# Performance work log

Measured on AMD Instinct MI355X. Metric: run time of the kernel, lower is better.

The kernel has to match this reference:

```python
import jax, jax.numpy as jnp
import numpy as np

B, N, DIN, DH, DOUT, H = 64, 512, 256, 512, 256, 4


def setup_inputs() -> dict:
    key = jax.random.key(0)
    ks = jax.random.split(key, 11)
    s = 0.02
    return {
        "x": jax.random.normal(ks[0], (B, N, DIN), jnp.float32),
        # block 0 (in=DIN): per-head embed Linear(DIN,DH) and KQ Linear(DIN,2*DH)
        "e_w0": jax.random.normal(ks[1], (H, DIN, DH), jnp.float32) * s,
        "e_b0": jax.random.normal(ks[2], (H, DH), jnp.float32) * s,
        "kq_w0": jax.random.normal(ks[3], (H, DIN, 2 * DH), jnp.float32) * s,
        "kq_b0": jax.random.normal(ks[4], (H, 2 * DH), jnp.float32) * s,
        # block 1 (in=DH)
        "e_w1": jax.random.normal(ks[5], (H, DH, DH), jnp.float32) * s,
        "e_b1": jax.random.normal(ks[6], (H, DH), jnp.float32) * s,
        "kq_w1": jax.random.normal(ks[7], (H, DH, 2 * DH), jnp.float32) * s,
        "kq_b1": jax.random.normal(ks[8], (H, 2 * DH), jnp.float32) * s,
        # output projection Linear(DH, DOUT)
        "proj_w": jax.random.normal(ks[9], (DH, DOUT), jnp.float32) * s,
        "proj_b": jax.random.normal(ks[10], (DOUT,), jnp.float32) * s,
    }


def _multi_attn(x, ew, eb, kqw, kqb):
    # x: [b,n,d]; ew: [h,d,e]; kqw: [h,d,2e]. num_hidden_layers=2 => each MLP is one Linear.
    embs = jnp.einsum('bnd,hde->hbne', x, ew) + eb[:, None, None, :]
    kq = jnp.einsum('bnd,hdf->hbnf', x, kqw) + kqb[:, None, None, :]
    K, Q = jnp.split(kq, 2, axis=-1)  # torch.chunk order: K first, then Q
    A = jax.nn.softmax(jnp.einsum('hbqe,hbke->hbqk', Q, K), axis=-1)  # unscaled
    out = jnp.einsum('hbqk,hbke->hbqe', A, embs)
    return out.mean(axis=0)  # mean over heads


def reference(x, e_w0, e_b0, kq_w0, kq_b0, e_w1, e_b1, kq_w1, kq_b1, proj_w, proj_b):
    h = _multi_attn(x, e_w0, e_b0, kq_w0, kq_b0)
    h = _multi_attn(h, e_w1, e_b1, kq_w1, kq_b1)
    return h @ proj_w + proj_b
```

## Files before the change

### kernel.cpp

```cpp
#include <hip/hip_runtime.h>

typedef _Float16 half8 __attribute__((ext_vector_type(8)));
typedef _Float16 half4 __attribute__((ext_vector_type(4)));
typedef float floatx4 __attribute__((ext_vector_type(4)));

#define B_    64
#define N_    512
#define DIN_  256
#define DH_   512
#define DOUT_ 256
#define H_    4
#define BN_   (B_ * N_)

#define WAIT_VM4_LGKM0() __builtin_amdgcn_s_waitcnt(0x0074)
#define WAIT_VM0_LGKM0() __builtin_amdgcn_s_waitcnt(0x0070)
#define WAIT_VM4()       __builtin_amdgcn_s_waitcnt(0x0F74)
#define WAIT_VM0()       __builtin_amdgcn_s_waitcnt(0x0F70)
#define MEMBAR()         __asm__ __volatile__("" ::: "memory")
#define BAR()            do { MEMBAR(); __builtin_amdgcn_s_barrier(); MEMBAR(); } while (0)

__device__ static inline void async_copy16(const _Float16* g, _Float16* l) {
    __builtin_amdgcn_global_load_lds(
        (const __attribute__((address_space(1))) void*)g,
        (__attribute__((address_space(3))) void*)l, 16, 0, 0);
}

template <bool OUT_F16>
__global__ __launch_bounds__(256)
void gemm_f16(const _Float16* __restrict__ A, long long aS1, long long aS2, int lda, long long aSeg,
              const _Float16* __restrict__ B, long long bS1, long long bS2, int ldb, long long bSeg,
              void* __restrict__ Cv, long long cS1, long long cS2, int ldc,
              int K, const float* __restrict__ bias, int biasMode,
              long long biasS1, long long biasS2, int zShift)
{
    __shared__ __align__(16) _Float16 As[3][128 * 32];
    __shared__ __align__(16) _Float16 Bs[3][128 * 32];

    const int tid  = threadIdx.x;
    const int wave = tid >> 6;
    const int lane = tid & 63;
    const int quad = lane >> 4;
    const int r16  = lane & 15;

    const int z  = blockIdx.z;
    const int z1 = z >> zShift;
    const int z2 = z & ((1 << zShift) - 1);

    const int gx = gridDim.x, gy = gridDim.y;
    const int T = gx * gy;
    int lin = blockIdx.y * gx + blockIdx.x;
    int id2 = (T & 7) ? lin : ((lin & 7) * (T >> 3) + (lin >> 3));
    const int m0 = (id2 / gx) * 128;
    const int n0 = (id2 % gx) * 128;

    const int srow = lane >> 2;
    const int scol = (((lane & 3) ^ ((lane >> 3) & 3))) * 8;

    const _Float16* gaRow = A + z1 * aS1 + z2 * aS2
                              + (long long)(m0 + wave * 32 + srow) * lda + scol;
    const _Float16* gbRow = B + z1 * bS1 + z2 * bS2
                              + (long long)(n0 + wave * 32 + srow) * ldb + scol;

    const int wm = (wave >> 1) * 64;
    const int wn = (wave & 1) * 64;
    const int gl = (quad ^ ((r16 >> 1) & 3)) * 8;

    floatx4 acc[4][4];
#pragma unroll
    for (int i = 0; i < 4; i++)
#pragma unroll
        for (int j = 0; j < 4; j++) acc[i][j] = (floatx4){0.f, 0.f, 0.f, 0.f};

    auto stage = [&](int p, int k0) {
        const _Float16* a = gaRow + (long long)(k0 >> 9) * aSeg + (k0 & 511);
        const _Float16* b = gbRow + (long long)(k0 >> 9) * bSeg + (k0 & 511);
        _Float16* la = &As[p][wave * 1024];
        _Float16* lb = &Bs[p][wave * 1024];
        async_copy16(a,                    la);
        async_copy16(a + (size_t)16 * lda, la + 512);
        async_copy16(b,                    lb);
        async_copy16(b + (size_t)16 * ldb, lb + 512);
    };

    auto compute = [&](int p) {
        half8 af[4], bf[4];
#pragma unroll
        for (int i = 0; i < 4; i++)
            af[i] = *(const half8*)&As[p][(wm + i * 16 + r16) * 32 + gl];
#pragma unroll
        for (int j = 0; j < 4; j++)
            bf[j] = *(const half8*)&Bs[p][(wn + j * 16 + r16) * 32 + gl];
#pragma unroll
        for (int i = 0; i < 4; i++)
#pragma unroll
            for (int j = 0; j < 4; j++)
                acc[i][j] = __builtin_amdgcn_mfma_f32_16x16x32_f16(
                    bf[j], af[i], acc[i][j], 0, 0, 0);
    };

    const int niter = K >> 5;
    stage(0, 0);
    stage(1, 32);
    int pNext = 2;
    int pCur  = 0;
    for (int it = 0; it < niter - 1; ++it) {
        MEMBAR(); WAIT_VM4_LGKM0();
        __builtin_amdgcn_s_barrier();
        MEMBAR();
        if (it + 2 < niter) stage(pNext, (it + 2) << 5);
        compute(pCur);
        MEMBAR();
        pNext = (pNext == 2) ? 0 : pNext + 1;
        pCur  = (pCur  == 2) ? 0 : pCur  + 1;
    }
    MEMBAR(); WAIT_VM0_LGKM0();
    __builtin_amdgcn_s_barrier(); MEMBAR();
    compute(pCur);

    const float* bz = bias + z1 * biasS1 + z2 * biasS2;
    float*    Cf = (float*)Cv    + z1 * cS1 + z2 * cS2;
    _Float16* Ch = (_Float16*)Cv + z1 * cS1 + z2 * cS2;
#pragma unroll
    for (int i = 0; i < 4; i++) {
        const int row = m0 + wm + i * 16 + r16;
#pragma unroll
        for (int j = 0; j < 4; j++) {
            const int col = n0 + wn + j * 16 + quad * 4;
            float v0 = acc[i][j][0], v1 = acc[i][j][1],
                  v2 = acc[i][j][2], v3 = acc[i][j][3];
            if (biasMode == 1) {
                v0 += bz[col]; v1 += bz[col + 1];
                v2 += bz[col + 2]; v3 += bz[col + 3];
            } else if (biasMode == 2) {
                const float bv = bz[row];
                v0 += bv; v1 += bv; v2 += bv; v3 += bv;
            }
            const size_t idx = (size_t)row * ldc + col;
            if (OUT_F16) {
                half4 hv = {(_Float16)v0, (_Float16)v1, (_Float16)v2, (_Float16)v3};
                *(half4*)&Ch[idx] = hv;
            } else {
                float4 fv = {v0, v1, v2, v3};
                *(float4*)&Cf[idx] = fv;
            }
        }
    }
}

template <bool OUT_F16>
__global__ __launch_bounds__(512, 2)
void gemm256(const _Float16* __restrict__ A, long long aS1, long long aS2, int lda, long long aSeg, int aSh,
             const _Float16* __restrict__ B, long long bS1, long long bS2, int ldb, long long bSeg, int bSh,
             void* __restrict__ Cv, long long cS1, long long cS2, int ldc,
             int K, const float* __restrict__ bias, int biasMode,
             long long biasS1, long long biasS2, int zShift)
{
    extern __shared__ __align__(16) _Float16 lds[];
    _Float16* AsB = lds;
    _Float16* BsB = lds + 2 * 256 * 64;

    const int tid  = threadIdx.x;
    const int wave = tid >> 6;
    const int lane = tid & 63;
    const int quad = lane >> 4;
    const int r16  = lane & 15;
    const int wr   = wave >> 2;
    const int wc   = wave & 3;

    const int z  = blockIdx.z;
    const int z1 = z >> zShift;
    const int z2 = z & ((1 << zShift) - 1);

    const int aTSh = aSh - 6, aTMk = (1 << aTSh) - 1;
    const int bTSh = bSh - 6, bTMk = (1 << bTSh) - 1;

    const int gx = gridDim.x, gy = gridDim.y;
    const int T = gx * gy;
    int lin = blockIdx.y * gx + blockIdx.x;
    int id2 = (T & 7) ? lin : ((lin & 7) * (T >> 3) + (lin >> 3));
    const int m0 = (id2 / gx) * 256;
    const int n0 = (id2 % gx) * 256;

    const int sr  = tid >> 3;
    const int swz = ((tid & 7) ^ (sr & 7)) * 8;
    const _Float16* gaA = A + z1 * aS1 + z2 * aS2 + (long long)(m0 + sr) * lda + swz;
    const _Float16* gbB = B + z1 * bS1 + z2 * bS2 + (long long)(n0 + sr) * ldb + swz;

    const int arow = wr * 64 + r16;
    const int brow = wc * 32 + r16;
    const int rsw  = r16 & 7;
    const int gxk0 = (quad ^ rsw) * 8;
    const int gxk1 = ((4 + quad) ^ rsw) * 8;

    floatx4 acc[8][4];
#pragma unroll
    for (int i = 0; i < 8; i++)
#pragma unroll
        for (int j = 0; j < 4; j++) acc[i][j] = (floatx4){0.f, 0.f, 0.f, 0.f};

    half8 af[4][2], bf0s[2][2], bf1s[2][2];

    auto stageA = [&](int buf, int h, int tt2) {
        const _Float16* s = gaA + (long long)(h * 128) * lda
                          + (long long)(tt2 >> aTSh) * aSeg + ((tt2 & aTMk) << 6);
        _Float16* d = AsB + buf * 16384 + h * 8192 + wave * 512;
        async_copy16(s, d);
        async_copy16(s + (long long)64 * lda, d + 4096);
    };
    auto stageB = [&](int buf, int h, int tt2) {
        const _Float16* s = gbB + (long long)(h * 128) * ldb
                          + (long long)(tt2 >> bTSh) * bSeg + ((tt2 & bTMk) << 6);
        _Float16* d = BsB + buf * 16384 + h * 8192 + wave * 512;
        async_copy16(s, d);
        async_copy16(s + (long long)64 * ldb, d + 4096);
    };

#define LOAD_AF(RH, BUF) do { \
    const _Float16* ab_ = AsB + (BUF) * 16384 + ((RH) * 128 + arow) * 64; \
    _Pragma("unroll") \
    for (int i5 = 0; i5 < 4; i5++) { \
        af[i5][0] = *(const half8*)(ab_ + i5 * 1024 + gxk0); \
        af[i5][1] = *(const half8*)(ab_ + i5 * 1024 + gxk1); \
    } \
} while (0)

#define LOAD_BF(DST, CH, BUF) do { \
    const _Float16* bb_ = BsB + (BUF) * 16384 + ((CH) * 128 + brow) * 64; \
    _Pragma("unroll") \
    for (int j5 = 0; j5 < 2; j5++) { \
        DST[j5][0] = *(const half8*)(bb_ + j5 * 1024 + gxk0); \
        DST[j5][1] = *(const half8*)(bb_ + j5 * 1024 + gxk1); \
    } \
} while (0)

#define MFMA16(RH, CH, BFS) do { \
    _Pragma("unroll") \
    for (int i6 = 0; i6 < 4; i6++) { \
        _Pragma("unroll") \
        for (int j6 = 0; j6 < 2; j6++) { \
            floatx4 c_ = acc[(RH) * 4 + i6][(CH) * 2 + j6]; \
            c_ = __builtin_amdgcn_mfma_f32_16x16x32_f16(BFS[j6][0], af[i6][0], c_, 0, 0, 0); \
            c_ = __builtin_amdgcn_mfma_f32_16x16x32_f16(BFS[j6][1], af[i6][1], c_, 0, 0, 0); \
            acc[(RH) * 4 + i6][(CH) * 2 + j6] = c_; \
        } \
    } \
} while (0)

    const int nit = K >> 7;

    stageA(0, 0, 0);
    stageB(0, 1, 0);
    stageA(0, 1, 0);
    stageB(0, 0, 0);
    stageA(1, 0, 1);
    stageB(1, 1, 1);
    WAIT_VM4();
    BAR();

    for (int it = 0; it < nit; ++it) {
        const int tt = it * 2;
        const bool full = (it < nit - 1);

        LOAD_AF(0, 0); LOAD_BF(bf0s, 0, 0);
        stageA(1, 1, tt + 1);
        BAR();
        __builtin_amdgcn_s_setprio(1); MFMA16(0, 0, bf0s); __builtin_amdgcn_s_setprio(0);
        BAR();
        LOAD_BF(bf1s, 1, 0);
        stageB(1, 0, tt + 1);
        BAR();
        __builtin_amdgcn_s_setprio(1); MFMA16(0, 1, bf1s); __builtin_amdgcn_s_setprio(0);
        BAR();
        LOAD_AF(1, 0);
        if (full) stageA(0, 0, tt + 2);
        BAR();
        __builtin_amdgcn_s_setprio(1); MFMA16(1, 1, bf1s); __builtin_amdgcn_s_setprio(0);
        BAR();
        if (full) stageB(0, 1, tt + 2);
        BAR();
        __builtin_amdgcn_s_setprio(1); MFMA16(1, 0, bf0s); __builtin_amdgcn_s_setprio(0);
        if (full) WAIT_VM4(); else WAIT_VM0();
        BAR();
        LOAD_AF(0, 1); LOAD_BF(bf0s, 0, 1);
        if (full) stageA(0, 1, tt + 2);
        BAR();
        __builtin_amdgcn_s_setprio(1); MFMA16(0, 0, bf0s); __builtin_amdgcn_s_setprio(0);
        BAR();
        LOAD_BF(bf1s, 1, 1);
        if (full) stageB(0, 0, tt + 2);
        BAR();
        __builtin_amdgcn_s_setprio(1); MFMA16(0, 1, bf1s); __builtin_amdgcn_s_setprio(0);
        BAR();
        LOAD_AF(1, 1);
        if (full) stageA(1, 0, tt + 3);
        BAR();
        __builtin_amdgcn_s_setprio(1); MFMA16(1, 1, bf1s); __builtin_amdgcn_s_setprio(0);
        BAR();
        if (full) stageB(1, 1, tt + 3);
        BAR();
        __builtin_amdgcn_s_setprio(1); MFMA16(1, 0, bf0s); __builtin_amdgcn_s_setprio(0);
        if (full) WAIT_VM4();
        BAR();
    }

#undef LOAD_AF
#undef LOAD_BF
#undef MFMA16

    const float* bz = bias + z1 * biasS1 + z2 * biasS2;
    float*    Cf = (float*)Cv    + z1 * cS1 + z2 * cS2;
    _Float16* Ch = (_Float16*)Cv + z1 * cS1 + z2 * cS2;
#pragma unroll
    for (int f = 0; f < 8; f++) {
        const int row = m0 + (f >> 2) * 128 + wr * 64 + (f & 3) * 16 + r16;
#pragma unroll
        for (int j = 0; j < 4; j++) {
            const int col = n0 + (j >> 1) * 128 + wc * 32 + (j & 1) * 16 + quad * 4;
            float v0 = acc[f][j][0], v1 = acc[f][j][1],
                  v2 = acc[f][j][2], v3 = acc[f][j][3];
            if (biasMode == 1) {
                v0 += bz[col]; v1 += bz[col + 1];
                v2 += bz[col + 2]; v3 += bz[col + 3];
            } else if (biasMode == 2) {
                const float bv = bz[row];
                v0 += bv; v1 += bv; v2 += bv; v3 += bv;
            }
            const size_t idx = (size_t)row * ldc + col;
            if (OUT_F16) {
                half4 hv = {(_Float16)v0, (_Float16)v1, (_Float16)v2, (_Float16)v3};
                *(half4*)&Ch[idx] = hv;
            } else {
                float4 fv = {v0, v1, v2, v3};
                *(float4*)&Cf[idx] = fv;
            }
        }
    }
}

__global__ __launch_bounds__(256)
void softmax_f16(_Float16* __restrict__ S)
{
    const int row  = blockIdx.x * 4 + (threadIdx.x >> 6);
    const int lane = threadIdx.x & 63;
    _Float16* s = S + (size_t)row * 512 + lane * 8;
    half8 h = *(const half8*)s;
    float v[8];
    float mx = -1e30f;
#pragma unroll
    for (int j = 0; j < 8; j++) { v[j] = (float)h[j]; mx = fmaxf(mx, v[j]); }
#pragma unroll
    for (int off = 32; off; off >>= 1) mx = fmaxf(mx, __shfl_xor(mx, off));
    float sum = 0.f;
#pragma unroll
    for (int j = 0; j < 8; j++) { v[j] = __expf(v[j] - mx); sum += v[j]; }
#pragma unroll
    for (int off = 32; off; off >>= 1) sum += __shfl_xor(sum, off);
    const float inv = 0.25f / sum;
#pragma unroll
    for (int j = 0; j < 8; j++) h[j] = (_Float16)(v[j] * inv);
    *(half8*)s = h;
}

__global__ __launch_bounds__(256)
void cvt_f32_f16(const float* __restrict__ in, _Float16* __restrict__ out)
{
    const size_t i = ((size_t)blockIdx.x * blockDim.x + threadIdx.x) * 4;
    const float4 f = *(const float4*)(in + i);
    out[i + 0] = (_Float16)f.x;
    out[i + 1] = (_Float16)f.y;
    out[i + 2] = (_Float16)f.z;
    out[i + 3] = (_Float16)f.w;
}

__global__ __launch_bounds__(256)
void transpose_cvt(const float* __restrict__ in, _Float16* __restrict__ out,
                   int R, int C)
{
    __shared__ float tile[32][33];
    const int g  = blockIdx.z;
    const int c0 = blockIdx.x * 32;
    const int r0 = blockIdx.y * 32;
    const float* inp  = in  + (size_t)g * R * C;
    _Float16*    outp = out + (size_t)g * R * C;
#pragma unroll
    for (int i = threadIdx.y; i < 32; i += 8)
        tile[i][threadIdx.x] = inp[(size_t)(r0 + i) * C + c0 + threadIdx.x];
    __syncthreads();
#pragma unroll
    for (int i = threadIdx.y; i < 32; i += 8)
        outp[(size_t)(c0 + i) * R + r0 + threadIdx.x] = (_Float16)tile[threadIdx.x][i];
}

__global__ __launch_bounds__(256)
void wk_bq(const float* __restrict__ kq_w, const float* __restrict__ kq_b,
           float* __restrict__ w, int dinShift)
{
    const int t = blockIdx.x * 256 + threadIdx.x;
    const int h = t >> dinShift;
    const int d = t & ((1 << dinShift) - 1);
    const float* wk = kq_w + ((size_t)(h << dinShift) + d) * (2 * DH_);
    const float* bq = kq_b + (size_t)h * 2 * DH_ + DH_;
    float s = 0.f;
    for (int e = 0; e < DH_; e++) s += wk[e] * bq[e];
    w[t] = s;
}

__global__ __launch_bounds__(256)
void fold_bias(const _Float16* __restrict__ projwT, const float* __restrict__ e_b1,
               float* __restrict__ be1p)
{
    const int t = blockIdx.x * 256 + threadIdx.x;
    const int h = t >> 8;
    const int o = t & 255;
    const _Float16* pw = projwT + (size_t)o * DH_;
    const float*    eb = e_b1 + (size_t)h * DH_;
    float s = 0.f;
    for (int d = 0; d < DH_; d++) s += (float)pw[d] * eb[d];
    be1p[t] = s;
}

__global__ __launch_bounds__(256)
void sum_b0(const float* __restrict__ eb, float* __restrict__ sb)
{
    const int e = blockIdx.x * 256 + threadIdx.x;
    sb[e] = 0.25f * (eb[e] + eb[DH_ + e] + eb[2 * DH_ + e] + eb[3 * DH_ + e]);
}

__global__ __launch_bounds__(256)
void compute_v(const _Float16* __restrict__ x, const float* __restrict__ w,
               float* __restrict__ V, int Kin)
{
    const int row  = blockIdx.x * 4 + (threadIdx.x >> 6);
    const int lane = threadIdx.x & 63;
    const int b = row >> 9, n = row & 511;
    const _Float16* xr = x + (size_t)row * Kin;
    float s0 = 0.f, s1 = 0.f, s2 = 0.f, s3 = 0.f;
    const int iters = Kin >> 6;
    for (int j = 0; j < iters; j++) {
        const int idx = lane + j * 64;
        const float xv = (float)xr[idx];
        s0 += xv * w[idx];
        s1 += xv * w[Kin + idx];
        s2 += xv * w[2 * Kin + idx];
        s3 += xv * w[3 * Kin + idx];
    }
#pragma unroll
    for (int off = 32; off; off >>= 1) {
        s0 += __shfl_xor(s0, off); s1 += __shfl_xor(s1, off);
        s2 += __shfl_xor(s2, off); s3 += __shfl_xor(s3, off);
    }
    if (lane == 0) {
        float* vb = V + ((size_t)b * H_) * N_ + n;
        vb[0] = s0; vb[N_] = s1; vb[2 * N_] = s2; vb[3 * N_] = s3;
    }
}

extern "C" void kernel_launch(void* const* d_in, const int* in_sizes, int n_in,
                              void* d_out, int out_size, void* d_ws, size_t ws_size,
                              hipStream_t stream)
{
    (void)in_sizes; (void)n_in; (void)out_size;

    static bool attr_set = false;
    if (!attr_set) {
        hipFuncSetAttribute((const void*)gemm256<true>,
                            hipFuncAttributeMaxDynamicSharedMemorySize, 131072);
        hipFuncSetAttribute((const void*)gemm256<false>,
                            hipFuncAttributeMaxDynamicSharedMemorySize, 131072);
        attr_set = true;
    }

    const float* x      = (const float*)d_in[0];
    const float* e_w0   = (const float*)d_in[1];
    const float* e_b0   = (const float*)d_in[2];
    const float* kq_w0  = (const float*)d_in[3];
    const float* kq_b0  = (const float*)d_in[4];
    const float* e_w1   = (const float*)d_in[5];
    const float* e_b1   = (const float*)d_in[6];
    const float* kq_w1  = (const float*)d_in[7];
    const float* kq_b1  = (const float*)d_in[8];
    const float* proj_w = (const float*)d_in[9];
    const float* proj_b = (const float*)d_in[10];
    float* out = (float*)d_out;

    char* ws = (char*)d_ws;
    size_t off = 0;
    auto alloc = [&](size_t bytes) -> char* {
        char* p = ws + off;
        off += (bytes + 255) & ~(size_t)255;
        return p;
    };

    _Float16* x16    = (_Float16*)alloc((size_t)BN_ * DIN_ * 2);
    _Float16* h1_16  = (_Float16*)alloc((size_t)BN_ * DH_ * 2);
    _Float16* ewT0   = (_Float16*)alloc((size_t)H_ * DH_ * DIN_ * 2);
    _Float16* projwT = (_Float16*)alloc((size_t)DOUT_ * DH_ * 2);
    _Float16* Mt0    = (_Float16*)alloc((size_t)H_ * DIN_ * DIN_ * 2);
    _Float16* Mt1    = (_Float16*)alloc((size_t)H_ * DH_ * DH_ * 2);
    _Float16* We1pT  = (_Float16*)alloc((size_t)H_ * DOUT_ * DH_ * 2);
    float*    be1p   = (float*)alloc((size_t)H_ * DOUT_ * 4);
    float*    w0     = (float*)alloc((size_t)H_ * DIN_ * 4);
    float*    w1     = (float*)alloc((size_t)H_ * DH_ * 4);
    float*    sb0    = (float*)alloc((size_t)DH_ * 4);
    float*    Vb     = (float*)alloc((size_t)B_ * H_ * N_ * 4);
    _Float16* xT     = (_Float16*)alloc((size_t)BN_ * DIN_ * 2);

    const size_t persistAll = off;
    const long long SB = (long long)N_ * N_;
    const size_t SC_FULL  = (size_t)B_ * H_ * N_ * N_ * 2;
    const size_t SC_CHUNK = SC_FULL / 2;
    const size_t A2_SZ    = (size_t)BN_ * H_ * DIN_ * 2;
    const size_t SLACK    = 1u << 20;

    const bool tierA = ws_size >= persistAll + SC_FULL + A2_SZ + SLACK;

    _Float16* Sc = (_Float16*)alloc(tierA ? SC_FULL : SC_CHUNK);
    _Float16* A2 = (_Float16*)alloc(A2_SZ);

    _Float16* kq0_16 = A2;
    _Float16* kq1_16 = kq0_16 + (size_t)H_ * DIN_ * 2 * DH_;
    _Float16* ew1_16 = kq1_16 + (size_t)H_ * DH_ * 2 * DH_;

    auto gemm = [&](bool outF16,
                    const _Float16* A, long long aS1, long long aS2, int lda, long long aSeg,
                    const _Float16* Bp, long long bS1, long long bS2, int ldb, long long bSeg,
                    void* C, long long cS1, long long cS2, int ldc,
                    int M, int Nn, int K, int batches, int zShift,
                    const float* bias, int biasMode, long long biasS1, long long biasS2,
                    int aSh, int bSh) {
        const bool can256 = (M % 256 == 0) && (Nn % 256 == 0) && (K % 128 == 0);
        const bool can128 = (M % 128 == 0) && (Nn % 128 == 0) && (K % 32 == 0)
                          && (aSh == 9) && (bSh == 9);
        const long long wg256 = can256 ? (long long)(M >> 8) * (Nn >> 8) * batches : 0;
        bool use256;
        if (!can128)            use256 = true;
        else if (!can256)       use256 = false;
        else                    use256 = (wg256 >= 192) || (wg256 >= 32 && wg256 * 4 < 128);
        if (use256) {
            dim3 grid(Nn / 256, M / 256, batches), block(512);
            if (outF16)
                gemm256<true><<<grid, block, 131072, stream>>>(A, aS1, aS2, lda, aSeg, aSh,
                    Bp, bS1, bS2, ldb, bSeg, bSh, C, cS1, cS2, ldc, K, bias, biasMode, biasS1, biasS2, zShift);
            else
                gemm256<false><<<grid, block, 131072, stream>>>(A, aS1, aS2, lda, aSeg, aSh,
                    Bp, bS1, bS2, ldb, bSeg, bSh, C, cS1, cS2, ldc, K, bias, biasMode, biasS1, biasS2, zShift);
        } else {
            dim3 grid(Nn / 128, M / 128, batches), block(256);
            if (outF16)
                gemm_f16<true><<<grid, block, 0, stream>>>(A, aS1, aS2, lda, aSeg,
                    Bp, bS1, bS2, ldb, bSeg, C, cS1, cS2, ldc, K, bias, biasMode, biasS1, biasS2, zShift);
            else
                gemm_f16<false><<<grid, block, 0, stream>>>(A, aS1, aS2, lda, aSeg,
                    Bp, bS1, bS2, ldb, bSeg, C, cS1, cS2, ldc, K, bias, biasMode, biasS1, biasS2, zShift);
        }
    };

    cvt_f32_f16<<<BN_ * DIN_ / 1024, 256, 0, stream>>>(x, x16);
    cvt_f32_f16<<<H_ * DIN_ * 2 * DH_ / 1024, 256, 0, stream>>>(kq_w0, kq0_16);
    cvt_f32_f16<<<H_ * DH_ * 2 * DH_ / 1024, 256, 0, stream>>>(kq_w1, kq1_16);
    cvt_f32_f16<<<H_ * DH_ * DH_ / 1024, 256, 0, stream>>>(e_w1, ew1_16);
    transpose_cvt<<<dim3(DH_ / 32, DIN_ / 32, H_), dim3(32, 8), 0, stream>>>(e_w0, ewT0, DIN_, DH_);
    transpose_cvt<<<dim3(DOUT_ / 32, DH_ / 32, 1), dim3(32, 8), 0, stream>>>(proj_w, projwT, DH_, DOUT_);
    transpose_cvt<<<dim3(DIN_ / 32, N_ / 32, B_), dim3(32, 8), 0, stream>>>(x, xT, N_, DIN_);
    sum_b0<<<DH_ / 256, 256, 0, stream>>>(e_b0, sb0);

    gemm(true, kq0_16, 0, (long long)DIN_ * 2 * DH_, 2 * DH_, 512,
         kq0_16 + DH_, 0, (long long)DIN_ * 2 * DH_, 2 * DH_, 512,
         Mt0, 0, (long long)DIN_ * DIN_, DIN_,
         DIN_, DIN_, DH_, H_, 2, nullptr, 0, 0, 0, 9, 9);
    gemm(true, kq1_16, 0, (long long)DH_ * 2 * DH_, 2 * DH_, 512,
         kq1_16 + DH_, 0, (long long)DH_ * 2 * DH_, 2 * DH_, 512,
         Mt1, 0, (long long)DH_ * DH_, DH_,
         DH_, DH_, DH_, H_, 2, nullptr, 0, 0, 0, 9, 9);
    gemm(true, projwT, 0, 0, DH_, 512,
         ew1_16, 0, (long long)DH_ * DH_, DH_, 512,
         We1pT, 0, (long long)DOUT_ * DH_, DH_,
         DOUT_, DH_, DH_, H_, 2, nullptr, 0, 0, 0, 9, 9);
    fold_bias<<<H_ * DOUT_ / 256, 256, 0, stream>>>(projwT, e_b1, be1p);
    wk_bq<<<H_ * DIN_ / 256, 256, 0, stream>>>(kq_w0, kq_b0, w0, 8);
    wk_bq<<<H_ * DH_ / 256, 256, 0, stream>>>(kq_w1, kq_b1, w1, 9);

    {
        const int CH0  = tierA ? B_ : 32;
        const int NCH0 = B_ / CH0;
        const size_t GCH = (size_t)CH0 * N_ * H_ * DIN_;
        compute_v<<<BN_ / 4, 256, 0, stream>>>(x16, w0, Vb, DIN_);
        for (int c = 0; c < NCH0; c++) {
            const _Float16* xc  = x16 + (size_t)c * CH0 * N_ * DIN_;
            const _Float16* xTc = xT  + (size_t)c * CH0 * DIN_ * N_;
            _Float16* slot = A2 + (size_t)c * GCH;
            gemm(true, xc, 0, 0, DIN_, 512,
                 Mt0, 0, 0, DIN_, 512,
                 slot, 0, 0, H_ * DIN_,
                 CH0 * N_, H_ * DIN_, DIN_, 1, 0, nullptr, 0, 0, 0, 9, 9);
            gemm(true, slot, (long long)N_ * H_ * DIN_, DIN_, H_ * DIN_, 512,
                 xc, (long long)N_ * DIN_, 0, DIN_, 512,
                 Sc, (long long)H_ * SB, SB, N_,
                 N_, N_, DIN_, CH0 * H_, 2,
                 Vb + (size_t)c * CH0 * H_ * N_, 1, (long long)H_ * N_, N_, 9, 9);
            softmax_f16<<<CH0 * H_ * N_ / 4, 256, 0, stream>>>(Sc);
            gemm(true, Sc, (long long)H_ * SB, SB, N_, 512,
                 xTc, (long long)DIN_ * N_, 0, N_, 512,
                 slot, (long long)H_ * N_ * DIN_, (long long)N_ * DIN_, DIN_,
                 N_, DIN_, N_, CH0 * H_, 2, nullptr, 0, 0, 0, 9, 9);
        }
        gemm(true, A2, (long long)H_ * N_ * DIN_, 0, DIN_, (long long)N_ * DIN_,
             ewT0, 0, 0, DIN_, (long long)DH_ * DIN_,
             h1_16, (long long)N_ * DH_, 0, DH_,
             N_, DH_, H_ * DIN_, B_, 0, sb0, 1, 0, 0, 8, 8);
    }

    {
        compute_v<<<BN_ / 4, 256, 0, stream>>>(h1_16, w1, Vb, DH_);
        for (int c = 0; c < 2; c++) {
            const _Float16* hc = h1_16 + (size_t)c * 32 * N_ * DH_;
            _Float16* Scp = tierA ? Sc + (size_t)c * 32 * H_ * SB : Sc;
            gemm(true, hc, 0, 0, DH_, 512,
                 Mt1, 0, 0, DH_, 512,
                 A2, 0, 0, H_ * DH_,
                 32 * N_, H_ * DH_, DH_, 1, 0, nullptr, 0, 0, 0, 9, 9);
            gemm(true, A2, (long long)N_ * H_ * DH_, DH_, H_ * DH_, 512,
                 hc, (long long)N_ * DH_, 0, DH_, 512,
                 Scp, (long long)H_ * SB, SB, N_,
                 N_, N_, DH_, 32 * H_, 2,
                 Vb + (size_t)c * 32 * H_ * N_, 1, (long long)H_ * N_, N_, 9, 9);
            softmax_f16<<<32 * H_ * N_ / 4, 256, 0, stream>>>(Scp);
            if (!tierA) {
                gemm(true, We1pT, 0, 0, DH_, 512,
                     hc, (long long)N_ * DH_, 0, DH_, 512,
                     A2, (long long)H_ * DOUT_ * N_, 0, N_,
                     H_ * DOUT_, N_, DH_, 32, 0, be1p, 2, 0, 0, 9, 9);
                gemm(false, Scp, (long long)H_ * SB, 0, N_, SB,
                     A2, (long long)H_ * DOUT_ * N_, 0, N_, (long long)DOUT_ * N_,
                     out + (size_t)c * 32 * N_ * DOUT_, (long long)N_ * DOUT_, 0, DOUT_,
                     N_, DOUT_, H_ * N_, 32, 0, proj_b, 1, 0, 0, 9, 9);
            }
        }
        if (tierA) {
            gemm(true, We1pT, 0, 0, DH_, 512,
                 h1_16, (long long)N_ * DH_, 0, DH_, 512,
                 A2, (long long)H_ * DOUT_ * N_, 0, N_,
                 H_ * DOUT_, N_, DH_, B_, 0, be1p, 2, 0, 0, 9, 9);
            gemm(false, Sc, (long long)H_ * SB, 0, N_, SB,
                 A2, (long long)H_ * DOUT_ * N_, 0, N_, (long long)DOUT_ * N_,
                 out, (long long)N_ * DOUT_, 0, DOUT_,
                 N_, DOUT_, H_ * N_, B_, 0, proj_b, 1, 0, 0, 9, 9);
        }
    }
}
```

Measured before the change: 989.0 us.

## Loop multiple batch slices per GEMM workgroup to keep prefetch pipeline running

Adds a zLoop parameter to the 256-tile GEMM so each workgroup handles several consecutive batch slices. Prefetching continues across slice boundaries, and a mid-loop epilogue writes and resets the accumulators after each slice. The score GEMMs use zLoop=2. The layer-1 Mt GEMM is reshaped into 64 batched 256-row slices, also with zLoop=2. The aim is to cut pipeline prologue and drain cost and launch tail effects, at the price of half as many workgroups and an epilogue inside the main loop.

```diff
diff --git a/kernel.cpp b/kernel.cpp
--- a/kernel.cpp
+++ b/kernel.cpp
@@ -153,7 +153,7 @@
              const _Float16* __restrict__ B, long long bS1, long long bS2, int ldb, long long bSeg, int bSh,
              void* __restrict__ Cv, long long cS1, long long cS2, int ldc,
              int K, const float* __restrict__ bias, int biasMode,
-             long long biasS1, long long biasS2, int zShift)
+             long long biasS1, long long biasS2, int zShift, int zLoop)
 {
     extern __shared__ __align__(16) _Float16 lds[];
     _Float16* AsB = lds;
@@ -167,24 +167,36 @@
     const int wr   = wave >> 2;
     const int wc   = wave & 3;
 
-    const int z  = blockIdx.z;
-    const int z1 = z >> zShift;
-    const int z2 = z & ((1 << zShift) - 1);
+    const int zBase = blockIdx.z * zLoop;
+    const int zMask = (1 << zShift) - 1;
 
     const int aTSh = aSh - 6, aTMk = (1 << aTSh) - 1;
     const int bTSh = bSh - 6, bTMk = (1 << bTSh) - 1;
 
+    const int ntiles = K >> 6;
+    const int ntSh   = __builtin_ctz(ntiles);
+    const int ntHMsk = (ntiles >> 1) - 1;
+    const int TTh    = (ntiles * zLoop) >> 1;
+
     const int gx = gridDim.x, gy = gridDim.y;
-    const int T = gx * gy;
+    const int T_ = gx * gy;
     int lin = blockIdx.y * gx + blockIdx.x;
-    int id2 = (T & 7) ? lin : ((lin & 7) * (T >> 3) + (lin >> 3));
+    int id2 = (T_ & 7) ? lin : ((lin & 7) * (T_ >> 3) + (lin >> 3));
     const int m0 = (id2 / gx) * 256;
     const int n0 = (id2 % gx) * 256;
 
     const int sr  = tid >> 3;
     const int swz = ((tid & 7) ^ (sr & 7)) * 8;
-    const _Float16* gaA = A + z1 * aS1 + z2 * aS2 + (long long)(m0 + sr) * lda + swz;
-    const _Float16* gbB = B + z1 * bS1 + z2 * bS2 + (long long)(n0 + sr) * ldb + swz;
+
+    const int zz0 = zBase, zz1 = zBase + (zLoop - 1);
+    const _Float16* gaA0 = A + (long long)(zz0 >> zShift) * aS1 + (long long)(zz0 & zMask) * aS2
+                             + (long long)(m0 + sr) * lda + swz;
+    const _Float16* gaA1 = A + (long long)(zz1 >> zShift) * aS1 + (long long)(zz1 & zMask) * aS2
+                             + (long long)(m0 + sr) * lda + swz;
+    const _Float16* gbB0 = B + (long long)(zz0 >> zShift) * bS1 + (long long)(zz0 & zMask) * bS2
+                             + (long long)(n0 + sr) * ldb + swz;
+    const _Float16* gbB1 = B + (long long)(zz1 >> zShift) * bS1 + (long long)(zz1 & zMask) * bS2
+                             + (long long)(n0 + sr) * ldb + swz;
 
     const int arow = wr * 64 + r16;
     const int brow = wc * 32 + r16;
@@ -200,19 +212,53 @@
 
     half8 af[4][2], bf0s[2][2], bf1s[2][2];
 
-    auto stageA = [&](int buf, int h, int tt2) {
-        const _Float16* s = gaA + (long long)(h * 128) * lda
-                          + (long long)(tt2 >> aTSh) * aSeg + ((tt2 & aTMk) << 6);
+    auto stageA = [&](int buf, int h, int T) {
+        const int tz = T >> ntSh, tk = T & (ntiles - 1);
+        const _Float16* s = (tz ? gaA1 : gaA0) + (long long)(h * 128) * lda
+                          + (long long)(tk >> aTSh) * aSeg + ((tk & aTMk) << 6);
         _Float16* d = AsB + buf * 16384 + h * 8192 + wave * 512;
         async_copy16(s, d);
         async_copy16(s + (long long)64 * lda, d + 4096);
     };
-    auto stageB = [&](int buf, int h, int tt2) {
-        const _Float16* s = gbB + (long long)(h * 128) * ldb
-                          + (long long)(tt2 >> bTSh) * bSeg + ((tt2 & bTMk) << 6);
+    auto stageB = [&](int buf, int h, int T) {
+        const int tz = T >> ntSh, tk = T & (ntiles - 1);
+        const _Float16* s = (tz ? gbB1 : gbB0) + (long long)(h * 128) * ldb
+                          + (long long)(tk >> bTSh) * bSeg + ((tk & bTMk) << 6);
         _Float16* d = BsB + buf * 16384 + h * 8192 + wave * 512;
         async_copy16(s, d);
         async_copy16(s + (long long)64 * ldb, d + 4096);
+    };
+
+    auto epi = [&](int zz) {
+        const int z1 = zz >> zShift, z2 = zz & zMask;
+        const float* bz = bias + (long long)z1 * biasS1 + (long long)z2 * biasS2;
+        float*    Cf = (float*)Cv    + (long long)z1 * cS1 + (long long)z2 * cS2;
+        _Float16* Ch = (_Float16*)Cv + (long long)z1 * cS1 + (long long)z2 * cS2;
+#pragma unroll
+        for (int f = 0; f < 8; f++) {
+            const int row = m0 + (f >> 2) * 128 + wr * 64 + (f & 3) * 16 + r16;
+#pragma unroll
+            for (int j = 0; j < 4; j++) {
+                const int col = n0 + (j >> 1) * 128 + wc * 32 + (j & 1) * 16 + quad * 4;
+                float v0 = acc[f][j][0], v1 = acc[f][j][1],
+                      v2 = acc[f][j][2], v3 = acc[f][j][3];
+                if (biasMode == 1) {
+                    v0 += bz[col]; v1 += bz[col + 1];
+                    v2 += bz[col + 2]; v3 += bz[col + 3];
+                } else if (biasMode == 2) {
+                    const float bv = bz[row];
+                    v0 += bv; v1 += bv; v2 += bv; v3 += bv;
+                }
+                const size_t idx = (size_t)row * ldc + col;
+                if (OUT_F16) {
+                    half4 hv = {(_Float16)v0, (_Float16)v1, (_Float16)v2, (_Float16)v3};
+                    *(half4*)&Ch[idx] = hv;
+                } else {
+                    float4 fv = {v0, v1, v2, v3};
+                    *(float4*)&Cf[idx] = fv;
+                }
+            }
+        }
     };
 
 #define LOAD_AF(RH, BUF) do { \
@@ -246,8 +292,6 @@
     } \
 } while (0)
 
-    const int nit = K >> 7;
-
     stageA(0, 0, 0);
     stageB(0, 1, 0);
     stageA(0, 1, 0);
@@ -257,84 +301,66 @@
     WAIT_VM4();
     BAR();
 
-    for (int it = 0; it < nit; ++it) {
-        const int tt = it * 2;
-        const bool full = (it < nit - 1);
+    int zi = 0;
+    for (int it = 0; it < TTh; ++it) {
+        const int T = it * 2;
+        const bool full = (it < TTh - 1);
 
         LOAD_AF(0, 0); LOAD_BF(bf0s, 0, 0);
-        stageA(1, 1, tt + 1);
+        stageA(1, 1, T + 1);
         BAR();
         __builtin_amdgcn_s_setprio(1); MFMA16(0, 0, bf0s); __builtin_amdgcn_s_setprio(0);
         BAR();
         LOAD_BF(bf1s, 1, 0);
-        stageB(1, 0, tt + 1);
+        stageB(1, 0, T + 1);
         BAR();
         __builtin_amdgcn_s_setprio(1); MFMA16(0, 1, bf1s); __builtin_amdgcn_s_setprio(0);
         BAR();
         LOAD_AF(1, 0);
-        if (full) stageA(0, 0, tt + 2);
+        if (full) stageA(0, 0, T + 2);
         BAR();
         __builtin_amdgcn_s_setprio(1); MFMA16(1, 1, bf1s); __builtin_amdgcn_s_setprio(0);
         BAR();
-        if (full) stageB(0, 1, tt + 2);
+        if (full) stageB(0, 1, T + 2);
         BAR();
         __builtin_amdgcn_s_setprio(1); MFMA16(1, 0, bf0s); __builtin_amdgcn_s_setprio(0);
         if (full) WAIT_VM4(); else WAIT_VM0();
         BAR();
         LOAD_AF(0, 1); LOAD_BF(bf0s, 0, 1);
-        if (full) stageA(0, 1, tt + 2);
+        if (full) stageA(0, 1, T + 2);
         BAR();
         __builtin_amdgcn_s_setprio(1); MFMA16(0, 0, bf0s); __builtin_amdgcn_s_setprio(0);
         BAR();
         LOAD_BF(bf1s, 1, 1);
-        if (full) stageB(0, 0, tt + 2);
+        if (full) stageB(0, 0, T + 2);
         BAR();
         __builtin_amdgcn_s_setprio(1); MFMA16(0, 1, bf1s); __builtin_amdgcn_s_setprio(0);
         BAR();
         LOAD_AF(1, 1);
-        if (full) stageA(1, 0, tt + 3);
+        if (full) stageA(1, 0, T + 3);
         BAR();
         __builtin_amdgcn_s_setprio(1); MFMA16(1, 1, bf1s); __builtin_amdgcn_s_setprio(0);
         BAR();
-        if (full) stageB(1, 1, tt + 3);
+        if (full) stageB(1, 1, T + 3);
         BAR();
         __builtin_amdgcn_s_setprio(1); MFMA16(1, 0, bf0s); __builtin_amdgcn_s_setprio(0);
         if (full) WAIT_VM4();
         BAR();
+
+        if (((it + 1) & ntHMsk) == 0) {
+            epi(zBase + zi);
+            ++zi;
+#pragma unroll
+            for (int i7 = 0; i7 < 8; i7++)
+#pragma unroll
+                for (int j7 = 0; j7 < 4; j7++)
+                    acc[i7][j7] = (floatx4){0.f, 0.f, 0.f, 0.f};
+        }
     }
 
 #undef LOAD_AF
 #undef LOAD_BF
 #undef MFMA16
-
-    const float* bz = bias + z1 * biasS1 + z2 * biasS2;
-    float*    Cf = (float*)Cv    + z1 * cS1 + z2 * cS2;
-    _Float16* Ch = (_Float16*)Cv + z1 * cS1 + z2 * cS2;
-#pragma unroll
-    for (int f = 0; f < 8; f++) {
-        const int row = m0 + (f >> 2) * 128 + wr * 64 + (f & 3) * 16 + r16;
-#pragma unroll
-        for (int j = 0; j < 4; j++) {
-            const int col = n0 + (j >> 1) * 128 + wc * 32 + (j & 1) * 16 + quad * 4;
-            float v0 = acc[f][j][0], v1 = acc[f][j][1],
-                  v2 = acc[f][j][2], v3 = acc[f][j][3];
-            if (biasMode == 1) {
-                v0 += bz[col]; v1 += bz[col + 1];
-                v2 += bz[col + 2]; v3 += bz[col + 3];
-            } else if (biasMode == 2) {
-                const float bv = bz[row];
-                v0 += bv; v1 += bv; v2 += bv; v3 += bv;
-            }
-            const size_t idx = (size_t)row * ldc + col;
-            if (OUT_F16) {
-                half4 hv = {(_Float16)v0, (_Float16)v1, (_Float16)v2, (_Float16)v3};
-                *(half4*)&Ch[idx] = hv;
-            } else {
-                float4 fv = {v0, v1, v2, v3};
-                *(float4*)&Cf[idx] = fv;
-            }
-        }
-    }
 }
 
 __global__ __launch_bounds__(256)
@@ -527,23 +553,24 @@
                     void* C, long long cS1, long long cS2, int ldc,
                     int M, int Nn, int K, int batches, int zShift,
                     const float* bias, int biasMode, long long biasS1, long long biasS2,
-                    int aSh, int bSh) {
+                    int aSh, int bSh, int zLoop) {
         const bool can256 = (M % 256 == 0) && (Nn % 256 == 0) && (K % 128 == 0);
         const bool can128 = (M % 128 == 0) && (Nn % 128 == 0) && (K % 32 == 0)
-                          && (aSh == 9) && (bSh == 9);
-        const long long wg256 = can256 ? (long long)(M >> 8) * (Nn >> 8) * batches : 0;
+                          && (aSh == 9) && (bSh == 9) && (zLoop == 1);
+        const long long wg256 = can256
+            ? (long long)(M >> 8) * (Nn >> 8) * (batches / zLoop) : 0;
         bool use256;
         if (!can128)            use256 = true;
         else if (!can256)       use256 = false;
         else                    use256 = (wg256 >= 192) || (wg256 >= 32 && wg256 * 4 < 128);
         if (use256) {
-            dim3 grid(Nn / 256, M / 256, batches), block(512);
+            dim3 grid(Nn / 256, M / 256, batches / zLoop), block(512);
             if (outF16)
                 gemm256<true><<<grid, block, 131072, stream>>>(A, aS1, aS2, lda, aSeg, aSh,
-                    Bp, bS1, bS2, ldb, bSeg, bSh, C, cS1, cS2, ldc, K, bias, biasMode, biasS1, biasS2, zShift);
+                    Bp, bS1, bS2, ldb, bSeg, bSh, C, cS1, cS2, ldc, K, bias, biasMode, biasS1, biasS2, zShift, zLoop);
             else
                 gemm256<false><<<grid, block, 131072, stream>>>(A, aS1, aS2, lda, aSeg, aSh,
-                    Bp, bS1, bS2, ldb, bSeg, bSh, C, cS1, cS2, ldc, K, bias, biasMode, biasS1, biasS2, zShift);
+                    Bp, bS1, bS2, ldb, bSeg, bSh, C, cS1, cS2, ldc, K, bias, biasMode, biasS1, biasS2, zShift, zLoop);
         } else {
             dim3 grid(Nn / 128, M / 128, batches), block(256);
             if (outF16)
@@ -567,15 +594,15 @@
     gemm(true, kq0_16, 0, (long long)DIN_ * 2 * DH_, 2 * DH_, 512,
          kq0_16 + DH_, 0, (long long)DIN_ * 2 * DH_, 2 * DH_, 512,
          Mt0, 0, (long long)DIN_ * DIN_, DIN_,
-         DIN_, DIN_, DH_, H_, 2, nullptr, 0, 0, 0, 9, 9);
+         DIN_, DIN_, DH_, H_, 2, nullptr, 0, 0, 0, 9, 9, 1);
     gemm(true, kq1_16, 0, (long long)DH_ * 2 * DH_, 2 * DH_, 512,
          kq1_16 + DH_, 0, (long long)DH_ * 2 * DH_, 2 * DH_, 512,
          Mt1, 0, (long long)DH_ * DH_, DH_,
-         DH_, DH_, DH_, H_, 2, nullptr, 0, 0, 0, 9, 9);
+         DH_, DH_, DH_, H_, 2, nullptr, 0, 0, 0, 9, 9, 1);
     gemm(true, projwT, 0, 0, DH_, 512,
          ew1_16, 0, (long long)DH_ * DH_, DH_, 512,
          We1pT, 0, (long long)DOUT_ * DH_, DH_,
-         DOUT_, DH_, DH_, H_, 2, nullptr, 0, 0, 0, 9, 9);
+         DOUT_, DH_, DH_, H_, 2, nullptr, 0, 0, 0, 9, 9, 1);
     fold_bias<<<H_ * DOUT_ / 256, 256, 0, stream>>>(projwT, e_b1, be1p);
     wk_bq<<<H_ * DIN_ / 256, 256, 0, stream>>>(kq_w0, kq_b0, w0, 8);
     wk_bq<<<H_ * DH_ / 256, 256, 0, stream>>>(kq_w1, kq_b1, w1, 9);
@@ -592,22 +619,22 @@
             gemm(true, xc, 0, 0, DIN_, 512,
                  Mt0, 0, 0, DIN_, 512,
                  slot, 0, 0, H_ * DIN_,
-                 CH0 * N_, H_ * DIN_, DIN_, 1, 0, nullptr, 0, 0, 0, 9, 9);
+                 CH0 * N_, H_ * DIN_, DIN_, 1, 0, nullptr, 0, 0, 0, 9, 9, 1);
             gemm(true, slot, (long long)N_ * H_ * DIN_, DIN_, H_ * DIN_, 512,
                  xc, (long long)N_ * DIN_, 0, DIN_, 512,
                  Sc, (long long)H_ * SB, SB, N_,
                  N_, N_, DIN_, CH0 * H_, 2,
-                 Vb + (size_t)c * CH0 * H_ * N_, 1, (long long)H_ * N_, N_, 9, 9);
+                 Vb + (size_t)c * CH0 * H_ * N_, 1, (long long)H_ * N_, N_, 9, 9, 2);
             softmax_f16<<<CH0 * H_ * N_ / 4, 256, 0, stream>>>(Sc);
             gemm(true, Sc, (long long)H_ * SB, SB, N_, 512,
                  xTc, (long long)DIN_ * N_, 0, N_, 512,
                  slot, (long long)H_ * N_ * DIN_, (long long)N_ * DIN_, DIN_,
-                 N_, DIN_, N_, CH0 * H_, 2, nullptr, 0, 0, 0, 9, 9);
+                 N_, DIN_, N_, CH0 * H_, 2, nullptr, 0, 0, 0, 9, 9, 1);
         }
         gemm(true, A2, (long long)H_ * N_ * DIN_, 0, DIN_, (long long)N_ * DIN_,
              ewT0, 0, 0, DIN_, (long long)DH_ * DIN_,
              h1_16, (long long)N_ * DH_, 0, DH_,
-             N_, DH_, H_ * DIN_, B_, 0, sb0, 1, 0, 0, 8, 8);
+             N_, DH_, H_ * DIN_, B_, 0, sb0, 1, 0, 0, 8, 8, 1);
     }
 
     {
@@ -615,36 +642,36 @@
         for (int c = 0; c < 2; c++) {
             const _Float16* hc = h1_16 + (size_t)c * 32 * N_ * DH_;
             _Float16* Scp = tierA ? Sc + (size_t)c * 32 * H_ * SB : Sc;
-            gemm(true, hc, 0, 0, DH_, 512,
+            gemm(true, hc, (long long)256 * DH_, 0, DH_, 512,
                  Mt1, 0, 0, DH_, 512,
-                 A2, 0, 0, H_ * DH_,
-                 32 * N_, H_ * DH_, DH_, 1, 0, nullptr, 0, 0, 0, 9, 9);
+                 A2, (long long)256 * H_ * DH_, 0, H_ * DH_,
+                 256, H_ * DH_, DH_, 64, 0, nullptr, 0, 0, 0, 9, 9, 2);
             gemm(true, A2, (long long)N_ * H_ * DH_, DH_, H_ * DH_, 512,
                  hc, (long long)N_ * DH_, 0, DH_, 512,
                  Scp, (long long)H_ * SB, SB, N_,
                  N_, N_, DH_, 32 * H_, 2,
-                 Vb + (size_t)c * 32 * H_ * N_, 1, (long long)H_ * N_, N_, 9, 9);
+                 Vb + (size_t)c * 32 * H_ * N_, 1, (long long)H_ * N_, N_, 9, 9, 2);
             softmax_f16<<<32 * H_ * N_ / 4, 256, 0, stream>>>(Scp);
             if (!tierA) {
                 gemm(true, We1pT, 0, 0, DH_, 512,
                      hc, (long long)N_ * DH_, 0, DH_, 512,
                      A2, (long long)H_ * DOUT_ * N_, 0, N_,
-                     H_ * DOUT_, N_, DH_, 32, 0, be1p, 2, 0, 0, 9, 9);
+                     H_ * DOUT_, N_, DH_, 32, 0, be1p, 2, 0, 0, 9, 9, 1);
                 gemm(false, Scp, (long long)H_ * SB, 0, N_, SB,
                      A2, (long long)H_ * DOUT_ * N_, 0, N_, (long long)DOUT_ * N_,
                      out + (size_t)c * 32 * N_ * DOUT_, (long long)N_ * DOUT_, 0, DOUT_,
-                     N_, DOUT_, H_ * N_, 32, 0, proj_b, 1, 0, 0, 9, 9);
+                     N_, DOUT_, H_ * N_, 32, 0, proj_b, 1, 0, 0, 9, 9, 1);
             }
         }
         if (tierA) {
             gemm(true, We1pT, 0, 0, DH_, 512,
                  h1_16, (long long)N_ * DH_, 0, DH_, 512,
                  A2, (long long)H_ * DOUT_ * N_, 0, N_,
-                 H_ * DOUT_, N_, DH_, B_, 0, be1p, 2, 0, 0, 9, 9);
+                 H_ * DOUT_, N_, DH_, B_, 0, be1p, 2, 0, 0, 9, 9, 1);
             gemm(false, Sc, (long long)H_ * SB, 0, N_, SB,
                  A2, (long long)H_ * DOUT_ * N_, 0, N_, (long long)DOUT_ * N_,
                  out, (long long)N_ * DOUT_, 0, DOUT_,
-                 N_, DOUT_, H_ * N_, B_, 0, proj_b, 1, 0, 0, 9, 9);
+                 N_, DOUT_, H_ * N_, B_, 0, proj_b, 1, 0, 0, 9, 9, 1);
         }
     }
 }
```

Result: faster. 965.5 us (-2.4%).
